# Performance work log

Measured on AMD Instinct MI355X. Metric: run time of the kernel, lower is better.

## Reference

```python
import jax, jax.numpy as jnp
import numpy as np

B, N, C = 4, 8192, 512
H, Dh, G, R = 8, 64, 64, 2  # heads, dim_head, slice_num, mlp_ratio
EPS_LN = 1e-5
EPS_NORM = 1e-5


def _ln(x, g, b):
    m = jnp.mean(x, axis=-1, keepdims=True)
    v = jnp.var(x, axis=-1, keepdims=True)
    return (x - m) * jax.lax.rsqrt(v + EPS_LN) * g + b


def setup_inputs() -> dict:
    key = jax.random.key(0)
    ks = jax.random.split(key, 16)
    r = lambda k, shp: jax.random.normal(k, shp, jnp.float32) * 0.02
    inner = H * Dh
    return {
        "fx": jax.random.normal(ks[0], (B, N, C), jnp.float32),
        "ln1_g": jnp.ones((C,), jnp.float32), "ln1_b": jnp.zeros((C,), jnp.float32),
        "Wx": r(ks[1], (C, inner)), "bx": jnp.zeros((inner,), jnp.float32),
        "Wfx": r(ks[2], (C, inner)), "bfx": jnp.zeros((inner,), jnp.float32),
        "Wslice": r(ks[3], (Dh, G)), "bslice": jnp.zeros((G,), jnp.float32),
        "temperature": jnp.full((1, H, 1, 1), 0.5, jnp.float32),
        "Wq": r(ks[4], (Dh, Dh)), "Wk": r(ks[5], (Dh, Dh)), "Wv": r(ks[6], (Dh, Dh)),
        "Wout": r(ks[7], (inner, C)), "bout": jnp.zeros((C,), jnp.float32),
        "tln_g": jnp.ones((Dh,), jnp.float32), "tln_b": jnp.zeros((Dh,), jnp.float32),
        "Wm1": r(ks[8], (Dh, R * Dh)), "bm1": jnp.zeros((R * Dh,), jnp.float32),
        "Wm2": r(ks[9], (R * Dh, Dh)), "bm2": jnp.zeros((Dh,), jnp.float32),
    }


def reference(fx, ln1_g, ln1_b, Wx, bx, Wfx, bfx, Wslice, bslice, temperature,
              Wq, Wk, Wv, Wout, bout, tln_g, tln_b, Wm1, bm1, Wm2, bm2):
    fx_norm = _ln(fx, ln1_g, ln1_b)                          # [B,N,C]
    # _forward_slice: project to per-head mid features
    x_mid = (fx_norm @ Wx + bx).reshape(B, N, H, Dh).transpose(0, 2, 1, 3)   # [B,H,N,Dh]
    fx_mid = (fx_norm @ Wfx + bfx).reshape(B, N, H, Dh).transpose(0, 2, 1, 3)
    # _project_token: soft slice assignment + weighted pooling into G tokens
    logits = jnp.einsum('bhnd,dg->bhng', x_mid, Wslice) + bslice
    slice_w = jax.nn.softmax(logits / temperature, axis=-1)  # [B,H,N,G]
    slice_norm = jnp.sum(slice_w, axis=2)                    # [B,H,G]
    slice_tok = jnp.einsum('bhnd,bhng->bhgd', fx_mid, slice_w) / (slice_norm[..., None] + EPS_NORM)
    # attention over the small token set (G tokens)
    q = slice_tok @ Wq
    k = slice_tok @ Wk
    v = slice_tok @ Wv
    scale = Dh ** -0.5
    attn = jax.nn.softmax(jnp.einsum('bhgd,bhpd->bhgp', q, k) * scale, axis=-1)
    out_tok = jnp.einsum('bhgp,bhpd->bhgd', attn, v) + slice_tok
    # token MLP with residual
    h = _ln(out_tok, tln_g, tln_b)
    h = jax.nn.gelu(h @ Wm1 + bm1, approximate=False) @ Wm2 + bm2
    tokens = h + out_tok                                     # [B,H,G,Dh]
    # _deslice: weighted scatter back to N points, merge heads, out projection
    out_x = jnp.einsum('bhgd,bhng->bhnd', tokens, slice_w)
    out_x = out_x.transpose(0, 2, 1, 3).reshape(B, N, H * Dh)
    out = out_x @ Wout + bout
    return out + fx_norm
```

## Files before the change

kernel.cpp:

```cpp
#include <hip/hip_runtime.h>
#include <math.h>

#define B_ 4
#define N_ 8192
#define C_ 512
#define H_ 8
#define M_ (B_ * N_)

typedef __attribute__((ext_vector_type(8))) short bf16x8;
typedef __attribute__((ext_vector_type(4))) float f32x4;
typedef __attribute__((ext_vector_type(8))) unsigned short u16x8;
typedef __attribute__((ext_vector_type(4))) unsigned short u16x4;

__device__ __forceinline__ float b2f(unsigned short u) {
  union { unsigned int i; float f; } v;
  v.i = ((unsigned int)u) << 16;
  return v.f;
}
__device__ __forceinline__ unsigned short f2b(float f) {
  union { float f; unsigned int i; } v;
  v.f = f;
  unsigned int r = v.i + 0x7fff + ((v.i >> 16) & 1);
  return (unsigned short)(r >> 16);
}
__device__ __forceinline__ void gl_lds16(const void* g, void* l) {
  __builtin_amdgcn_global_load_lds(
      (const __attribute__((address_space(1))) unsigned int*)g,
      (__attribute__((address_space(3))) unsigned int*)l, 16, 0, 0);
}

__global__ __launch_bounds__(256) void ln_bf16(
    const float* __restrict__ x, const float* __restrict__ gam,
    const float* __restrict__ bet, unsigned short* __restrict__ y) {
  int wave = threadIdx.x >> 6, lane = threadIdx.x & 63;
  int row = (blockIdx.x << 2) + wave;
  const float4* xr = (const float4*)(x + (size_t)row * C_);
  float4 v0 = xr[lane], v1 = xr[lane + 64];
  float s = v0.x + v0.y + v0.z + v0.w + v1.x + v1.y + v1.z + v1.w;
  float q = v0.x * v0.x + v0.y * v0.y + v0.z * v0.z + v0.w * v0.w +
            v1.x * v1.x + v1.y * v1.y + v1.z * v1.z + v1.w * v1.w;
#pragma unroll
  for (int off = 32; off; off >>= 1) {
    s += __shfl_xor(s, off);
    q += __shfl_xor(q, off);
  }
  float mean = s * (1.0f / C_);
  float var = q * (1.0f / C_) - mean * mean;
  float rstd = rsqrtf(var + 1e-5f);
  const float4* gr = (const float4*)gam;
  const float4* br = (const float4*)bet;
  float4 g0 = gr[lane], g1 = gr[lane + 64];
  float4 b0 = br[lane], b1 = br[lane + 64];
  u16x4 oa, ob;
  oa.x = f2b((v0.x - mean) * rstd * g0.x + b0.x);
  oa.y = f2b((v0.y - mean) * rstd * g0.y + b0.y);
  oa.z = f2b((v0.z - mean) * rstd * g0.z + b0.z);
  oa.w = f2b((v0.w - mean) * rstd * g0.w + b0.w);
  ob.x = f2b((v1.x - mean) * rstd * g1.x + b1.x);
  ob.y = f2b((v1.y - mean) * rstd * g1.y + b1.y);
  ob.z = f2b((v1.z - mean) * rstd * g1.z + b1.z);
  ob.w = f2b((v1.w - mean) * rstd * g1.w + b1.w);
  unsigned short* yr = y + (size_t)row * C_;
  *(u16x4*)(yr + (lane << 2)) = oa;
  *(u16x4*)(yr + 256 + (lane << 2)) = ob;
}

__global__ __launch_bounds__(256) void wconv_t(const float* __restrict__ W,
                                               unsigned short* __restrict__ Wt) {
  __shared__ float tile[64][65];
  int t = threadIdx.x;
  int r0 = (int)blockIdx.y << 6, c0 = (int)blockIdx.x << 6;
  int lr = t >> 4, lc = (t & 15) << 2;
#pragma unroll
  for (int p = 0; p < 4; p++) {
    float4 v = *(const float4*)(W + (size_t)(r0 + lr + p * 16) * 512 + c0 + lc);
    tile[lr + p * 16][lc + 0] = v.x;
    tile[lr + p * 16][lc + 1] = v.y;
    tile[lr + p * 16][lc + 2] = v.z;
    tile[lr + p * 16][lc + 3] = v.w;
  }
  __syncthreads();
  int on = t >> 2, ok = (t & 3) << 4;
  unsigned short tmp[16];
#pragma unroll
  for (int j = 0; j < 16; j++) tmp[j] = f2b(tile[ok + j][on]);
  unsigned short* op = Wt + (size_t)(c0 + on) * 512 + r0 + ok;
#pragma unroll
  for (int j4 = 0; j4 < 4; j4++) *(u16x4*)(op + (j4 << 2)) = *(u16x4*)(tmp + (j4 << 2));
}

__global__ __launch_bounds__(256) void wslice_prep(const float* __restrict__ Ws,
                                                   unsigned short* __restrict__ wf) {
  int t = threadIdx.x;
#pragma unroll
  for (int i = 0; i < 2; i++) {
    int idx = t + i * 256;
    int f = idx >> 6, l = idx & 63;
    int gt = f >> 1, ks = f & 1;
    int g = (gt << 4) + (l & 15);
    int d0 = (ks << 5) + ((l >> 4) << 3);
    unsigned short v[8];
#pragma unroll
    for (int jj = 0; jj < 8; jj++) v[jj] = f2b(Ws[(size_t)(d0 + jj) * 64 + g]);
    *(u16x4*)(wf + idx * 8) = *(u16x4*)v;
    *(u16x4*)(wf + idx * 8 + 4) = *(u16x4*)(v + 4);
  }
}

__global__ __launch_bounds__(256) void wfrag_prep(
    const float* __restrict__ Wq, const float* __restrict__ Wk,
    const float* __restrict__ Wv, const float* __restrict__ Wm1,
    const float* __restrict__ Wm2, unsigned short* __restrict__ wfr) {
  int t = threadIdx.x;
  for (int task = t; task < 56 * 64; task += 256) {
    int fid = task >> 6, l = task & 63;
    const float* W;
    int stride, ct, ks;
    if (fid < 24) {
      W = (fid < 8) ? Wq : (fid < 16) ? Wk : Wv;
      int e = fid & 7;
      ct = e >> 1;
      ks = e & 1;
      stride = 64;
    } else if (fid < 40) {
      W = Wm1;
      int e = fid - 24;
      ct = e >> 1;
      ks = e & 1;
      stride = 128;
    } else {
      W = Wm2;
      int e = fid - 40;
      ct = e >> 2;
      ks = e & 3;
      stride = 64;
    }
    int d0 = (ks << 5) + ((l >> 4) << 3);
    int c = (ct << 4) + (l & 15);
    unsigned short v[8];
#pragma unroll
    for (int j = 0; j < 8; j++) v[j] = f2b(W[(size_t)(d0 + j) * stride + c]);
    *(u16x4*)(wfr + task * 8) = *(u16x4*)v;
    *(u16x4*)(wfr + task * 8 + 4) = *(u16x4*)(v + 4);
  }
}

__global__ __launch_bounds__(256) void tokfrag_prep(
    const float* __restrict__ tokens, unsigned short* __restrict__ wtokf) {
  int bh = blockIdx.x, t = threadIdx.x, w = t >> 6, l = t & 63;
  const float* tp = tokens + ((size_t)bh << 12);
#pragma unroll
  for (int fid = w; fid < 8; fid += 4) {
    int mt = fid >> 1, ks = fid & 1;
    int d = (mt << 4) + (l & 15);
    int g0 = (ks << 5) + ((l >> 4) << 3);
    unsigned short v[8];
#pragma unroll
    for (int j = 0; j < 8; j++) v[j] = f2b(tp[(g0 + j) * 64 + d]);
    unsigned short* op = wtokf + (((size_t)bh << 3) + fid) * 512 + (l << 3);
    *(u16x4*)op = *(u16x4*)v;
    *(u16x4*)(op + 4) = *(u16x4*)(v + 4);
  }
}

template <int DEC, bool BIASROW, bool OUTBF, bool RES>
__global__ __launch_bounds__(256) void gemm_bf16(
    const unsigned short* __restrict__ A, const unsigned short* __restrict__ Bt,
    const float* __restrict__ bias, const unsigned short* __restrict__ resid,
    void* __restrict__ Cout, size_t ldC) {
  __shared__ unsigned short lds[8192];
  const int t = threadIdx.x;
  const int w = t >> 6, l = t & 63;
  int bid = blockIdx.x;
  int xcd = bid & 7, q = bid >> 3;
  int bm, bn;
  if (DEC == 0) {
    bm = ((xcd << 5) + (q >> 2)) << 7;
    bn = (q & 3) << 7;
  } else {
    bn = ((xcd << 5) + (q >> 2)) << 7;
    bm = (q & 3) << 7;
  }
  const int wm = (w >> 1) << 6, wn = (w & 1) << 6;
  f32x4 acc[4][4];
#pragma unroll
  for (int mt = 0; mt < 4; mt++)
#pragma unroll
    for (int nt = 0; nt < 4; nt++) acc[mt][nt] = (f32x4){0.f, 0.f, 0.f, 0.f};

  const int srow = t >> 2;
  const int scol = (t & 3) << 3;
  const unsigned short* gA0 = A + (size_t)(bm + srow) * 512 + scol;
  const unsigned short* gA1 = A + (size_t)(bm + 64 + srow) * 512 + scol;
  const unsigned short* gB0 = Bt + (size_t)(bn + srow) * 512 + scol;
  const unsigned short* gB1 = Bt + (size_t)(bn + 64 + srow) * 512 + scol;
  const int fr = l & 15, fq = (l >> 4) << 3;

  for (int k0 = 0; k0 < 512; k0 += 32) {
    gl_lds16(gA0 + k0, lds + (w << 9));
    gl_lds16(gA1 + k0, lds + 2048 + (w << 9));
    gl_lds16(gB0 + k0, lds + 4096 + (w << 9));
    gl_lds16(gB1 + k0, lds + 6144 + (w << 9));
    __syncthreads();
    bf16x8 af[4], bfr[4];
#pragma unroll
    for (int mt = 0; mt < 4; mt++)
      af[mt] = *(const bf16x8*)&lds[(wm + mt * 16 + fr) * 32 + fq];
#pragma unroll
    for (int nt = 0; nt < 4; nt++)
      bfr[nt] = *(const bf16x8*)&lds[4096 + (wn + nt * 16 + fr) * 32 + fq];
#pragma unroll
    for (int mt = 0; mt < 4; mt++)
#pragma unroll
      for (int nt = 0; nt < 4; nt++)
        acc[mt][nt] = __builtin_amdgcn_mfma_f32_16x16x32_bf16(
            af[mt], bfr[nt], acc[mt][nt], 0, 0, 0);
    __syncthreads();
  }

  const int col0 = bn + wn + (l & 15);
  const int row0 = bm + wm + ((l >> 4) << 2);
#pragma unroll
  for (int mt = 0; mt < 4; mt++) {
#pragma unroll
    for (int j = 0; j < 4; j++) {
      int row = row0 + mt * 16 + j;
#pragma unroll
      for (int nt = 0; nt < 4; nt++) {
        int col = col0 + nt * 16;
        float v = acc[mt][nt][j] + (BIASROW ? bias[row] : bias[col]);
        if (RES) v += b2f(resid[(size_t)row * ldC + col]);
        if (OUTBF)
          ((unsigned short*)Cout)[(size_t)row * ldC + col] = f2b(v);
        else
          ((float*)Cout)[(size_t)row * ldC + col] = v;
      }
    }
  }
}

__global__ __launch_bounds__(256) void slice_mfma(
    unsigned short* __restrict__ xw, const unsigned short* __restrict__ wf,
    const float* __restrict__ bslice, const float* __restrict__ temp) {
  __shared__ unsigned short xs[4096];
  int t = threadIdx.x, w = t >> 6, l = t & 63;
  int blk = blockIdx.x;
  size_t base = (size_t)blk << 12;
  {
    int srow = t >> 2;
    const unsigned short* gp = xw + base + srow * 64 + ((t & 3) << 4);
    u16x8 a = *(const u16x8*)gp;
    u16x8 b = *(const u16x8*)(gp + 8);
    int sl0 = (t & 3) << 1, swz = srow & 7;
    *(u16x8*)&xs[srow * 64 + ((sl0 ^ swz) << 3)] = a;
    *(u16x8*)&xs[srow * 64 + (((sl0 + 1) ^ swz) << 3)] = b;
  }
  bf16x8 wsf[4][2];
#pragma unroll
  for (int gt = 0; gt < 4; gt++)
#pragma unroll
    for (int ks = 0; ks < 2; ks++)
      wsf[gt][ks] = *(const bf16x8*)(wf + (((gt << 1) + ks) * 64 + l) * 8);
  __syncthreads();

  int xr = (w << 4) + (l & 15);
  f32x4 acc[4];
#pragma unroll
  for (int gt = 0; gt < 4; gt++) acc[gt] = (f32x4){0.f, 0.f, 0.f, 0.f};
#pragma unroll
  for (int ks = 0; ks < 2; ks++) {
    int slot = (ks << 2) + (l >> 4);
    bf16x8 xf = *(const bf16x8*)&xs[xr * 64 + ((slot ^ (xr & 7)) << 3)];
#pragma unroll
    for (int gt = 0; gt < 4; gt++)
      acc[gt] = __builtin_amdgcn_mfma_f32_16x16x32_bf16(wsf[gt][ks], xf,
                                                        acc[gt], 0, 0, 0);
  }

  int gxr = (blk << 6) + xr;
  float invt = 1.0f / temp[gxr & 7];
  int qq = l >> 4;
  float lg[16];
  float mx = -1e30f;
#pragma unroll
  for (int gt = 0; gt < 4; gt++)
#pragma unroll
    for (int r = 0; r < 4; r++) {
      float v = (acc[gt][r] + bslice[(gt << 4) + (qq << 2) + r]) * invt;
      lg[(gt << 2) + r] = v;
      mx = fmaxf(mx, v);
    }
  mx = fmaxf(mx, __shfl_xor(mx, 16));
  mx = fmaxf(mx, __shfl_xor(mx, 32));
  float ssum = 0.f;
#pragma unroll
  for (int i = 0; i < 16; i++) {
    lg[i] = expf(lg[i] - mx);
    ssum += lg[i];
  }
  ssum += __shfl_xor(ssum, 16);
  ssum += __shfl_xor(ssum, 32);
  float inv = 1.0f / ssum;
  __syncthreads();
#pragma unroll
  for (int gt = 0; gt < 4; gt++) {
    int slot = (gt << 1) + (qq >> 1);
    int off = ((slot ^ (xr & 7)) << 3) + ((qq & 1) << 2);
    u16x4 pk;
    pk.x = f2b(lg[(gt << 2) + 0] * inv);
    pk.y = f2b(lg[(gt << 2) + 1] * inv);
    pk.z = f2b(lg[(gt << 2) + 2] * inv);
    pk.w = f2b(lg[(gt << 2) + 3] * inv);
    *(u16x4*)&xs[xr * 64 + off] = pk;
  }
  __syncthreads();
  {
    int rr = (w << 4) + (l >> 2);
    int sl = (l & 3) << 1, swz = rr & 7;
    u16x8 o0 = *(const u16x8*)&xs[rr * 64 + ((sl ^ swz) << 3)];
    u16x8 o1 = *(const u16x8*)&xs[rr * 64 + (((sl + 1) ^ swz) << 3)];
    unsigned short* op = xw + base + rr * 64 + ((l & 3) << 4);
    *(u16x8*)op = o0;
    *(u16x8*)(op + 8) = o1;
  }
}

__global__ __launch_bounds__(256) void pool_mfma(
    const unsigned short* __restrict__ sw, const unsigned short* __restrict__ fxT,
    float* __restrict__ tok_part, float* __restrict__ norm_part) {
  __shared__ unsigned short wT[4096];
  int bid = blockIdx.x;
  int bh = bid >> 4, c = bid & 15;
  int b = bh >> 3, h = bh & 7;
  int t = threadIdx.x, w = t >> 6, l = t & 63;
  int n0 = c << 9;
  const int fr15 = l & 15, fs = l >> 4;
  f32x4 acc[4];
#pragma unroll
  for (int gt = 0; gt < 4; gt++) acc[gt] = (f32x4){0.f, 0.f, 0.f, 0.f};
  float nacc[4] = {0.f, 0.f, 0.f, 0.f};

  const unsigned short* fxrow =
      fxT + (size_t)(h * 64 + w * 16 + fr15) * 32768 + b * N_ + n0 + (fs << 3);

  for (int nn = 0; nn < 512; nn += 64) {
    size_t srow = ((size_t)(b * N_ + n0 + nn + l) * 8 + h) << 6;
    u16x8 a0 = *(const u16x8*)(sw + srow + w * 16);
    u16x8 a1 = *(const u16x8*)(sw + srow + w * 16 + 8);
    __syncthreads();
#pragma unroll
    for (int j = 0; j < 16; j++) {
      int g = (w << 4) + j;
      unsigned short v = (j < 8) ? (unsigned short)a0[j] : (unsigned short)a1[j - 8];
      wT[(g << 6) + (((l >> 3) ^ (g & 7)) << 3) + (l & 7)] = v;
    }
    __syncthreads();
#pragma unroll
    for (int kk = 0; kk < 2; kk++) {
      bf16x8 bfrag = *(const bf16x8*)(fxrow + nn + (kk << 5));
#pragma unroll
      for (int gt = 0; gt < 4; gt++) {
        int g = (gt << 4) + fr15;
        int slot = (kk << 2) + fs;
        bf16x8 af = *(const bf16x8*)&wT[(g << 6) + ((slot ^ (g & 7)) << 3)];
        acc[gt] = __builtin_amdgcn_mfma_f32_16x16x32_bf16(af, bfrag, acc[gt], 0, 0, 0);
        if (w == 0) {
#pragma unroll
          for (int j = 0; j < 8; j++) nacc[gt] += b2f((unsigned short)af[j]);
        }
      }
    }
  }
  float* op = tok_part + ((size_t)bid << 12);
#pragma unroll
  for (int gt = 0; gt < 4; gt++)
#pragma unroll
    for (int rr = 0; rr < 4; rr++)
      op[((gt << 4) + (fs << 2) + rr) * 64 + (w << 4) + fr15] = acc[gt][rr];
  if (w == 0) {
#pragma unroll
    for (int gt = 0; gt < 4; gt++) {
      float s = nacc[gt];
      s += __shfl_xor(s, 16);
      s += __shfl_xor(s, 32);
      if (l < 16) norm_part[(bid << 6) + (gt << 4) + l] = s;
    }
  }
}

__global__ __launch_bounds__(256) void tok_reduce(
    const float* __restrict__ tok_part, const float* __restrict__ norm_part,
    float* __restrict__ stG) {
  int blk = blockIdx.x;
  int bh = blk >> 2, qq = blk & 3;
  int t = threadIdx.x;
  int e = (qq << 10) + (t << 2);
  int g = e >> 6;
  float s = 0.f;
  const float* np = norm_part + ((size_t)bh << 10);
#pragma unroll
  for (int c = 0; c < 16; c++) s += np[(c << 6) + g];
  float4 acc = make_float4(0.f, 0.f, 0.f, 0.f);
  const float* tp = tok_part + ((size_t)bh << 16) + e;
#pragma unroll
  for (int c = 0; c < 16; c++) {
    float4 v = *(const float4*)(tp + (c << 12));
    acc.x += v.x;
    acc.y += v.y;
    acc.z += v.z;
    acc.w += v.w;
  }
  float inv = 1.0f / (s + 1e-5f);
  acc.x *= inv;
  acc.y *= inv;
  acc.z *= inv;
  acc.w *= inv;
  *(float4*)(stG + ((size_t)bh << 12) + e) = acc;
}

__device__ __forceinline__ float gelu_exact(float x) {
  return 0.5f * x * (1.0f + erff(x * 0.70710678118654752f));
}

__global__ __launch_bounds__(256) void token_mfma(
    const float* __restrict__ stG, const unsigned short* __restrict__ wfr,
    const float* __restrict__ tg, const float* __restrict__ tb,
    const float* __restrict__ bm1, const float* __restrict__ bm2,
    float* __restrict__ tokens) {
  __shared__ __align__(16) char smem[54272];
  unsigned short* stb = (unsigned short*)smem;
  float* st32 = (float*)(smem + 9216);
  unsigned short* hmld = (unsigned short*)(smem + 9216);
  unsigned short* qld = (unsigned short*)(smem + 26624);
  unsigned short* kld = (unsigned short*)(smem + 35840);
  unsigned short* vtl = (unsigned short*)(smem + 45056);

  int bh = blockIdx.x, t = threadIdx.x, w = t >> 6, l = t & 63;
  const int fr = l & 15, fq = l >> 4;

  {
    int r = t >> 2, c0 = (t & 3) << 4;
    const float* gp = stG + ((size_t)bh << 12) + r * 64 + c0;
    float4 a = *(const float4*)gp;
    float4 b = *(const float4*)(gp + 4);
    float4 c = *(const float4*)(gp + 8);
    float4 d = *(const float4*)(gp + 12);
    *(float4*)&st32[r * 68 + c0] = a;
    *(float4*)&st32[r * 68 + c0 + 4] = b;
    *(float4*)&st32[r * 68 + c0 + 8] = c;
    *(float4*)&st32[r * 68 + c0 + 12] = d;
    unsigned short tv[16];
    tv[0] = f2b(a.x); tv[1] = f2b(a.y); tv[2] = f2b(a.z); tv[3] = f2b(a.w);
    tv[4] = f2b(b.x); tv[5] = f2b(b.y); tv[6] = f2b(b.z); tv[7] = f2b(b.w);
    tv[8] = f2b(c.x); tv[9] = f2b(c.y); tv[10] = f2b(c.z); tv[11] = f2b(c.w);
    tv[12] = f2b(d.x); tv[13] = f2b(d.y); tv[14] = f2b(d.z); tv[15] = f2b(d.w);
    *(u16x8*)&stb[r * 72 + c0] = *(u16x8*)tv;
    *(u16x8*)&stb[r * 72 + c0 + 8] = *(u16x8*)(tv + 8);
  }
  __syncthreads();

  const int orow = (w << 4) + (fq << 2);

  {
    bf16x8 af[2];
#pragma unroll
    for (int ks = 0; ks < 2; ks++)
      af[ks] = *(const bf16x8*)&stb[((w << 4) + fr) * 72 + (ks << 5) + (fq << 3)];
    f32x4 aq[4], ak[4], av[4];
#pragma unroll
    for (int ct = 0; ct < 4; ct++) {
      aq[ct] = (f32x4){0.f, 0.f, 0.f, 0.f};
      ak[ct] = (f32x4){0.f, 0.f, 0.f, 0.f};
      av[ct] = (f32x4){0.f, 0.f, 0.f, 0.f};
    }
#pragma unroll
    for (int ct = 0; ct < 4; ct++)
#pragma unroll
      for (int ks = 0; ks < 2; ks++) {
        bf16x8 bq = *(const bf16x8*)&wfr[(((ct << 1) + ks) * 64 + l) * 8];
        aq[ct] = __builtin_amdgcn_mfma_f32_16x16x32_bf16(af[ks], bq, aq[ct], 0, 0, 0);
      }
#pragma unroll
    for (int ct = 0; ct < 4; ct++)
#pragma unroll
      for (int ks = 0; ks < 2; ks++) {
        bf16x8 bk = *(const bf16x8*)&wfr[((8 + (ct << 1) + ks) * 64 + l) * 8];
        ak[ct] = __builtin_amdgcn_mfma_f32_16x16x32_bf16(af[ks], bk, ak[ct], 0, 0, 0);
      }
#pragma unroll
    for (int ct = 0; ct < 4; ct++)
#pragma unroll
      for (int ks = 0; ks < 2; ks++) {
        bf16x8 bv = *(const bf16x8*)&wfr[((16 + (ct << 1) + ks) * 64 + l) * 8];
        av[ct] = __builtin_amdgcn_mfma_f32_16x16x32_bf16(af[ks], bv, av[ct], 0, 0, 0);
      }
#pragma unroll
    for (int ct = 0; ct < 4; ct++) {
#pragma unroll
      for (int rr = 0; rr < 4; rr++) {
        qld[(orow + rr) * 72 + (ct << 4) + fr] = f2b(aq[ct][rr]);
        kld[(orow + rr) * 72 + (ct << 4) + fr] = f2b(ak[ct][rr]);
      }
      u16x4 vp;
      vp.x = f2b(av[ct][0]);
      vp.y = f2b(av[ct][1]);
      vp.z = f2b(av[ct][2]);
      vp.w = f2b(av[ct][3]);
      *(u16x4*)&vtl[((ct << 4) + fr) * 72 + orow] = vp;
    }
  }
  __syncthreads();

  {
    bf16x8 aq[2];
#pragma unroll
    for (int ks = 0; ks < 2; ks++)
      aq[ks] = *(const bf16x8*)&qld[((w << 4) + fr) * 72 + (ks << 5) + (fq << 3)];
    f32x4 accs[4];
#pragma unroll
    for (int nt = 0; nt < 4; nt++) accs[nt] = (f32x4){0.f, 0.f, 0.f, 0.f};
#pragma unroll
    for (int nt = 0; nt < 4; nt++)
#pragma unroll
      for (int ks = 0; ks < 2; ks++) {
        bf16x8 bk = *(const bf16x8*)&kld[((nt << 4) + fr) * 72 + (ks << 5) + (fq << 3)];
        accs[nt] = __builtin_amdgcn_mfma_f32_16x16x32_bf16(aq[ks], bk, accs[nt], 0, 0, 0);
      }
#pragma unroll
    for (int rr = 0; rr < 4; rr++) {
      float v0 = accs[0][rr] * 0.125f, v1 = accs[1][rr] * 0.125f;
      float v2 = accs[2][rr] * 0.125f, v3 = accs[3][rr] * 0.125f;
      float mx = fmaxf(fmaxf(v0, v1), fmaxf(v2, v3));
      mx = fmaxf(mx, __shfl_xor(mx, 1));
      mx = fmaxf(mx, __shfl_xor(mx, 2));
      mx = fmaxf(mx, __shfl_xor(mx, 4));
      mx = fmaxf(mx, __shfl_xor(mx, 8));
      float e0 = expf(v0 - mx), e1 = expf(v1 - mx);
      float e2 = expf(v2 - mx), e3 = expf(v3 - mx);
      float ss = e0 + e1 + e2 + e3;
      ss += __shfl_xor(ss, 1);
      ss += __shfl_xor(ss, 2);
      ss += __shfl_xor(ss, 4);
      ss += __shfl_xor(ss, 8);
      float inv = 1.0f / ss;
      stb[(orow + rr) * 72 + 0 * 16 + fr] = f2b(e0 * inv);
      stb[(orow + rr) * 72 + 1 * 16 + fr] = f2b(e1 * inv);
      stb[(orow + rr) * 72 + 2 * 16 + fr] = f2b(e2 * inv);
      stb[(orow + rr) * 72 + 3 * 16 + fr] = f2b(e3 * inv);
    }
  }
  __syncthreads();

  float o16[4][4];
  {
    bf16x8 ap[2];
#pragma unroll
    for (int ks = 0; ks < 2; ks++)
      ap[ks] = *(const bf16x8*)&stb[((w << 4) + fr) * 72 + (ks << 5) + (fq << 3)];
    f32x4 acco[4];
#pragma unroll
    for (int ct = 0; ct < 4; ct++) acco[ct] = (f32x4){0.f, 0.f, 0.f, 0.f};
#pragma unroll
    for (int ct = 0; ct < 4; ct++)
#pragma unroll
      for (int ks = 0; ks < 2; ks++) {
        bf16x8 bv = *(const bf16x8*)&vtl[((ct << 4) + fr) * 72 + (ks << 5) + (fq << 3)];
        acco[ct] = __builtin_amdgcn_mfma_f32_16x16x32_bf16(ap[ks], bv, acco[ct], 0, 0, 0);
      }
    float tgv[4], tbv[4];
#pragma unroll
    for (int ct = 0; ct < 4; ct++) {
      tgv[ct] = tg[(ct << 4) + fr];
      tbv[ct] = tb[(ct << 4) + fr];
    }
#pragma unroll
    for (int ct = 0; ct < 4; ct++)
#pragma unroll
      for (int rr = 0; rr < 4; rr++)
        o16[ct][rr] = acco[ct][rr] + st32[(orow + rr) * 68 + (ct << 4) + fr];
#pragma unroll
    for (int rr = 0; rr < 4; rr++) {
      float sm = o16[0][rr] + o16[1][rr] + o16[2][rr] + o16[3][rr];
      float sq = o16[0][rr] * o16[0][rr] + o16[1][rr] * o16[1][rr] +
                 o16[2][rr] * o16[2][rr] + o16[3][rr] * o16[3][rr];
      sm += __shfl_xor(sm, 1);
      sm += __shfl_xor(sm, 2);
      sm += __shfl_xor(sm, 4);
      sm += __shfl_xor(sm, 8);
      sq += __shfl_xor(sq, 1);
      sq += __shfl_xor(sq, 2);
      sq += __shfl_xor(sq, 4);
      sq += __shfl_xor(sq, 8);
      float mean = sm * (1.0f / 64.0f);
      float var = sq * (1.0f / 64.0f) - mean * mean;
      float rstd = rsqrtf(var + 1e-5f);
#pragma unroll
      for (int ct = 0; ct < 4; ct++) {
        float hv = (o16[ct][rr] - mean) * rstd * tgv[ct] + tbv[ct];
        qld[(orow + rr) * 72 + (ct << 4) + fr] = f2b(hv);
      }
    }
  }
  __syncthreads();

  {
    bf16x8 ah[2];
#pragma unroll
    for (int ks = 0; ks < 2; ks++)
      ah[ks] = *(const bf16x8*)&qld[((w << 4) + fr) * 72 + (ks << 5) + (fq << 3)];
    f32x4 accm[8];
#pragma unroll
    for (int et = 0; et < 8; et++) accm[et] = (f32x4){0.f, 0.f, 0.f, 0.f};
#pragma unroll
    for (int et = 0; et < 8; et++)
#pragma unroll
      for (int ks = 0; ks < 2; ks++) {
        bf16x8 bm = *(const bf16x8*)&wfr[((24 + (et << 1) + ks) * 64 + l) * 8];
        accm[et] = __builtin_amdgcn_mfma_f32_16x16x32_bf16(ah[ks], bm, accm[et], 0, 0, 0);
      }
#pragma unroll
    for (int et = 0; et < 8; et++) {
      float bv = bm1[(et << 4) + fr];
#pragma unroll
      for (int rr = 0; rr < 4; rr++) {
        float x = accm[et][rr] + bv;
        hmld[(orow + rr) * 136 + (et << 4) + fr] = f2b(gelu_exact(x));
      }
    }
  }
  __syncthreads();

  {
    bf16x8 ahm[4];
#pragma unroll
    for (int ks = 0; ks < 4; ks++)
      ahm[ks] = *(const bf16x8*)&hmld[((w << 4) + fr) * 136 + (ks << 5) + (fq << 3)];
    f32x4 acc2[4];
#pragma unroll
    for (int ct = 0; ct < 4; ct++) acc2[ct] = (f32x4){0.f, 0.f, 0.f, 0.f};
#pragma unroll
    for (int ct = 0; ct < 4; ct++)
#pragma unroll
      for (int ks = 0; ks < 4; ks++) {
        bf16x8 bw = *(const bf16x8*)&wfr[((40 + (ct << 2) + ks) * 64 + l) * 8];
        acc2[ct] = __builtin_amdgcn_mfma_f32_16x16x32_bf16(ahm[ks], bw, acc2[ct], 0, 0, 0);
      }
    float* tout = tokens + ((size_t)bh << 12);
#pragma unroll
    for (int ct = 0; ct < 4; ct++) {
      float bv = bm2[(ct << 4) + fr];
#pragma unroll
      for (int rr = 0; rr < 4; rr++)
        tout[(orow + rr) * 64 + (ct << 4) + fr] = acc2[ct][rr] + bv + o16[ct][rr];
    }
  }
}

__global__ __launch_bounds__(256) void deslice_mfma(
    const unsigned short* __restrict__ wtokf, const unsigned short* __restrict__ sw,
    unsigned short* __restrict__ outx) {
  int bid = blockIdx.x;
  int bh = bid >> 4, c = bid & 15;
  int b = bh >> 3, h = bh & 7;
  int t = threadIdx.x, w = t >> 6, l = t & 63;
  const int fr = l & 15, fq = l >> 4;

  bf16x8 ta[4][2];
  const unsigned short* fp = wtokf + ((size_t)bh << 12);
#pragma unroll
  for (int mt = 0; mt < 4; mt++)
#pragma unroll
    for (int ks = 0; ks < 2; ks++)
      ta[mt][ks] = *(const bf16x8*)(fp + (((mt << 1) + ks) << 9) + (l << 3));

  int n0 = (c << 9) + (w << 7);
#pragma unroll 2
  for (int ntile = 0; ntile < 8; ntile++) {
    int nb = n0 + (ntile << 4);
    size_t rowb = ((size_t)(b * N_ + nb + fr) * 8 + h) << 6;
    bf16x8 b0 = *(const bf16x8*)(sw + rowb + (fq << 3));
    bf16x8 b1 = *(const bf16x8*)(sw + rowb + 32 + (fq << 3));
    f32x4 acc[4];
#pragma unroll
    for (int mt = 0; mt < 4; mt++) acc[mt] = (f32x4){0.f, 0.f, 0.f, 0.f};
#pragma unroll
    for (int mt = 0; mt < 4; mt++) {
      acc[mt] = __builtin_amdgcn_mfma_f32_16x16x32_bf16(ta[mt][0], b0, acc[mt], 0, 0, 0);
      acc[mt] = __builtin_amdgcn_mfma_f32_16x16x32_bf16(ta[mt][1], b1, acc[mt], 0, 0, 0);
    }
    unsigned short* op = outx + rowb + (fq << 2);
#pragma unroll
    for (int mt = 0; mt < 4; mt++) {
      u16x4 pk;
      pk.x = f2b(acc[mt][0]);
      pk.y = f2b(acc[mt][1]);
      pk.z = f2b(acc[mt][2]);
      pk.w = f2b(acc[mt][3]);
      *(u16x4*)(op + (mt << 4)) = pk;
    }
  }
}

extern "C" void kernel_launch(void* const* d_in, const int* in_sizes, int n_in,
                              void* d_out, int out_size, void* d_ws,
                              size_t ws_size, hipStream_t stream) {
  const float* fx = (const float*)d_in[0];
  const float* ln1g = (const float*)d_in[1];
  const float* ln1b = (const float*)d_in[2];
  const float* Wx = (const float*)d_in[3];
  const float* bx = (const float*)d_in[4];
  const float* Wfx = (const float*)d_in[5];
  const float* bfx = (const float*)d_in[6];
  const float* Wsl = (const float*)d_in[7];
  const float* bsl = (const float*)d_in[8];
  const float* temp = (const float*)d_in[9];
  const float* Wq = (const float*)d_in[10];
  const float* Wk = (const float*)d_in[11];
  const float* Wv = (const float*)d_in[12];
  const float* Wout = (const float*)d_in[13];
  const float* bout = (const float*)d_in[14];
  const float* tlng = (const float*)d_in[15];
  const float* tlnb = (const float*)d_in[16];
  const float* Wm1 = (const float*)d_in[17];
  const float* bm1 = (const float*)d_in[18];
  const float* Wm2 = (const float*)d_in[19];
  const float* bm2 = (const float*)d_in[20];
  float* out = (float*)d_out;

  char* p = (char*)d_ws;
  const size_t MC2 = (size_t)M_ * 512 * 2;
  unsigned short* fxn = (unsigned short*)p;  p += MC2;
  unsigned short* buf1 = (unsigned short*)p; p += MC2;
  unsigned short* bufT = (unsigned short*)p; p += MC2;
  unsigned short* WtX = (unsigned short*)p;  p += 512 * 512 * 2;
  unsigned short* WtF = (unsigned short*)p;  p += 512 * 512 * 2;
  unsigned short* WtO = (unsigned short*)p;  p += 512 * 512 * 2;
  unsigned short* wsf = (unsigned short*)p;  p += 8192;
  unsigned short* wfr = (unsigned short*)p;  p += 56 * 512 * 2;
  unsigned short* wtokf = (unsigned short*)p; p += (size_t)32 * 8 * 512 * 2;
  float* tok_part = (float*)p;  p += (size_t)512 * 4096 * 4;
  float* norm_part = (float*)p; p += (size_t)512 * 64 * 4;
  float* tokens = (float*)p;    p += (size_t)32 * 4096 * 4;
  float* stG = (float*)p;       p += (size_t)32 * 4096 * 4;

  ln_bf16<<<M_ / 4, 256, 0, stream>>>(fx, ln1g, ln1b, fxn);
  dim3 wg(8, 8);
  wconv_t<<<wg, 256, 0, stream>>>(Wx, WtX);
  wconv_t<<<wg, 256, 0, stream>>>(Wfx, WtF);
  wconv_t<<<wg, 256, 0, stream>>>(Wout, WtO);
  wslice_prep<<<1, 256, 0, stream>>>(Wsl, wsf);
  wfrag_prep<<<1, 256, 0, stream>>>(Wq, Wk, Wv, Wm1, Wm2, wfr);
  gemm_bf16<0, false, true, false><<<1024, 256, 0, stream>>>(fxn, WtX, bx, nullptr, buf1, 512);
  gemm_bf16<1, true, true, false><<<1024, 256, 0, stream>>>(WtF, fxn, bfx, nullptr, bufT, 32768);
  slice_mfma<<<4096, 256, 0, stream>>>(buf1, wsf, bsl, temp);
  pool_mfma<<<512, 256, 0, stream>>>(buf1, bufT, tok_part, norm_part);
  tok_reduce<<<128, 256, 0, stream>>>(tok_part, norm_part, stG);
  token_mfma<<<32, 256, 0, stream>>>(stG, wfr, tlng, tlnb, bm1, bm2, tokens);
  tokfrag_prep<<<32, 256, 0, stream>>>(tokens, wtokf);
  deslice_mfma<<<512, 256, 0, stream>>>(wtokf, buf1, bufT);
  gemm_bf16<0, false, false, true><<<1024, 256, 0, stream>>>(bufT, WtO, bout, fxn, out, 512);
}
```

Before: 192.9 us.

## Fuse slice softmax into x-projection GEMM, double-buffer GEMM LDS, merge prep kernels

Merges the five weight-preparation launches into a single prep_all kernel. Adds double-buffered LDS staging to the bf16 GEMM so the next K tile is loaded while MFMAs run on the current one. Fuses the slice-logit MFMA and softmax into the epilogue of the x-projection GEMM, so x_mid is never written to and re-read from global memory. In exchange, LDS use per block doubles, which may lower occupancy, and the fused epilogue adds register pressure.

```diff
diff --git a/kernel.cpp b/kernel.cpp
--- a/kernel.cpp
+++ b/kernel.cpp
@@ -65,83 +65,84 @@
   *(u16x4*)(yr + 256 + (lane << 2)) = ob;
 }
 
-__global__ __launch_bounds__(256) void wconv_t(const float* __restrict__ W,
-                                               unsigned short* __restrict__ Wt) {
-  __shared__ float tile[64][65];
-  int t = threadIdx.x;
-  int r0 = (int)blockIdx.y << 6, c0 = (int)blockIdx.x << 6;
-  int lr = t >> 4, lc = (t & 15) << 2;
-#pragma unroll
-  for (int p = 0; p < 4; p++) {
-    float4 v = *(const float4*)(W + (size_t)(r0 + lr + p * 16) * 512 + c0 + lc);
-    tile[lr + p * 16][lc + 0] = v.x;
-    tile[lr + p * 16][lc + 1] = v.y;
-    tile[lr + p * 16][lc + 2] = v.z;
-    tile[lr + p * 16][lc + 3] = v.w;
-  }
-  __syncthreads();
-  int on = t >> 2, ok = (t & 3) << 4;
-  unsigned short tmp[16];
-#pragma unroll
-  for (int j = 0; j < 16; j++) tmp[j] = f2b(tile[ok + j][on]);
-  unsigned short* op = Wt + (size_t)(c0 + on) * 512 + r0 + ok;
-#pragma unroll
-  for (int j4 = 0; j4 < 4; j4++) *(u16x4*)(op + (j4 << 2)) = *(u16x4*)(tmp + (j4 << 2));
-}
-
-__global__ __launch_bounds__(256) void wslice_prep(const float* __restrict__ Ws,
-                                                   unsigned short* __restrict__ wf) {
-  int t = threadIdx.x;
-#pragma unroll
-  for (int i = 0; i < 2; i++) {
-    int idx = t + i * 256;
-    int f = idx >> 6, l = idx & 63;
-    int gt = f >> 1, ks = f & 1;
-    int g = (gt << 4) + (l & 15);
-    int d0 = (ks << 5) + ((l >> 4) << 3);
-    unsigned short v[8];
-#pragma unroll
-    for (int jj = 0; jj < 8; jj++) v[jj] = f2b(Ws[(size_t)(d0 + jj) * 64 + g]);
-    *(u16x4*)(wf + idx * 8) = *(u16x4*)v;
-    *(u16x4*)(wf + idx * 8 + 4) = *(u16x4*)(v + 4);
-  }
-}
-
-__global__ __launch_bounds__(256) void wfrag_prep(
+__global__ __launch_bounds__(256) void prep_all(
+    const float* __restrict__ Wx, const float* __restrict__ Wfx,
+    const float* __restrict__ Wout, const float* __restrict__ Wsl,
     const float* __restrict__ Wq, const float* __restrict__ Wk,
     const float* __restrict__ Wv, const float* __restrict__ Wm1,
-    const float* __restrict__ Wm2, unsigned short* __restrict__ wfr) {
-  int t = threadIdx.x;
-  for (int task = t; task < 56 * 64; task += 256) {
-    int fid = task >> 6, l = task & 63;
-    const float* W;
-    int stride, ct, ks;
-    if (fid < 24) {
-      W = (fid < 8) ? Wq : (fid < 16) ? Wk : Wv;
-      int e = fid & 7;
-      ct = e >> 1;
-      ks = e & 1;
-      stride = 64;
-    } else if (fid < 40) {
-      W = Wm1;
-      int e = fid - 24;
-      ct = e >> 1;
-      ks = e & 1;
-      stride = 128;
-    } else {
-      W = Wm2;
-      int e = fid - 40;
-      ct = e >> 2;
-      ks = e & 3;
-      stride = 64;
-    }
-    int d0 = (ks << 5) + ((l >> 4) << 3);
-    int c = (ct << 4) + (l & 15);
-    unsigned short v[8];
-#pragma unroll
-    for (int j = 0; j < 8; j++) v[j] = f2b(W[(size_t)(d0 + j) * stride + c]);
-    *(u16x4*)(wfr + task * 8) = *(u16x4*)v;
-    *(u16x4*)(wfr + task * 8 + 4) = *(u16x4*)(v + 4);
+    const float* __restrict__ Wm2, unsigned short* __restrict__ WtX,
+    unsigned short* __restrict__ WtF, unsigned short* __restrict__ WtO,
+    unsigned short* __restrict__ wsf, unsigned short* __restrict__ wfr) {
+  __shared__ float tile[64][65];
+  int blk = blockIdx.x, t = threadIdx.x;
+  if (blk < 192) {
+    int which = blk >> 6, sub = blk & 63;
+    const float* W = (which == 0) ? Wx : (which == 1) ? Wfx : Wout;
+    unsigned short* Wt = (which == 0) ? WtX : (which == 1) ? WtF : WtO;
+    int r0 = (sub >> 3) << 6, c0 = (sub & 7) << 6;
+    int lr = t >> 4, lc = (t & 15) << 2;
+#pragma unroll
+    for (int p = 0; p < 4; p++) {
+      float4 v = *(const float4*)(W + (size_t)(r0 + lr + p * 16) * 512 + c0 + lc);
+      tile[lr + p * 16][lc + 0] = v.x;
+      tile[lr + p * 16][lc + 1] = v.y;
+      tile[lr + p * 16][lc + 2] = v.z;
+      tile[lr + p * 16][lc + 3] = v.w;
+    }
+    __syncthreads();
+    int on = t >> 2, ok = (t & 3) << 4;
+    unsigned short tmp[16];
+#pragma unroll
+    for (int j = 0; j < 16; j++) tmp[j] = f2b(tile[ok + j][on]);
+    unsigned short* op = Wt + (size_t)(c0 + on) * 512 + r0 + ok;
+#pragma unroll
+    for (int j4 = 0; j4 < 4; j4++)
+      *(u16x4*)(op + (j4 << 2)) = *(u16x4*)(tmp + (j4 << 2));
+  } else {
+#pragma unroll
+    for (int i = 0; i < 2; i++) {
+      int idx = t + i * 256;
+      int f = idx >> 6, l = idx & 63;
+      int gt = f >> 1, ks = f & 1;
+      int g = (gt << 4) + (l & 15);
+      int d0 = (ks << 5) + ((l >> 4) << 3);
+      unsigned short v[8];
+#pragma unroll
+      for (int jj = 0; jj < 8; jj++) v[jj] = f2b(Wsl[(size_t)(d0 + jj) * 64 + g]);
+      *(u16x4*)(wsf + idx * 8) = *(u16x4*)v;
+      *(u16x4*)(wsf + idx * 8 + 4) = *(u16x4*)(v + 4);
+    }
+    for (int task = t; task < 56 * 64; task += 256) {
+      int fid = task >> 6, l = task & 63;
+      const float* W;
+      int stride, ct, ks;
+      if (fid < 24) {
+        W = (fid < 8) ? Wq : (fid < 16) ? Wk : Wv;
+        int e = fid & 7;
+        ct = e >> 1;
+        ks = e & 1;
+        stride = 64;
+      } else if (fid < 40) {
+        W = Wm1;
+        int e = fid - 24;
+        ct = e >> 1;
+        ks = e & 1;
+        stride = 128;
+      } else {
+        W = Wm2;
+        int e = fid - 40;
+        ct = e >> 2;
+        ks = e & 3;
+        stride = 64;
+      }
+      int d0 = (ks << 5) + ((l >> 4) << 3);
+      int c = (ct << 4) + (l & 15);
+      unsigned short v[8];
+#pragma unroll
+      for (int j = 0; j < 8; j++) v[j] = f2b(W[(size_t)(d0 + j) * stride + c]);
+      *(u16x4*)(wfr + task * 8) = *(u16x4*)v;
+      *(u16x4*)(wfr + task * 8 + 4) = *(u16x4*)(v + 4);
+    }
   }
 }
 
@@ -168,7 +169,7 @@
     const unsigned short* __restrict__ A, const unsigned short* __restrict__ Bt,
     const float* __restrict__ bias, const unsigned short* __restrict__ resid,
     void* __restrict__ Cout, size_t ldC) {
-  __shared__ unsigned short lds[8192];
+  __shared__ unsigned short lds[16384];
   const int t = threadIdx.x;
   const int w = t >> 6, l = t & 63;
   int bid = blockIdx.x;
@@ -196,19 +197,29 @@
   const unsigned short* gB1 = Bt + (size_t)(bn + 64 + srow) * 512 + scol;
   const int fr = l & 15, fq = (l >> 4) << 3;
 
-  for (int k0 = 0; k0 < 512; k0 += 32) {
-    gl_lds16(gA0 + k0, lds + (w << 9));
-    gl_lds16(gA1 + k0, lds + 2048 + (w << 9));
-    gl_lds16(gB0 + k0, lds + 4096 + (w << 9));
-    gl_lds16(gB1 + k0, lds + 6144 + (w << 9));
-    __syncthreads();
+  gl_lds16(gA0, lds + (w << 9));
+  gl_lds16(gA1, lds + 2048 + (w << 9));
+  gl_lds16(gB0, lds + 4096 + (w << 9));
+  gl_lds16(gB1, lds + 6144 + (w << 9));
+  __syncthreads();
+  int cur = 0;
+  for (int ks = 0; ks < 16; ks++) {
+    if (ks < 15) {
+      int k0 = (ks + 1) << 5;
+      unsigned short* st = lds + ((cur ^ 1) << 13);
+      gl_lds16(gA0 + k0, st + (w << 9));
+      gl_lds16(gA1 + k0, st + 2048 + (w << 9));
+      gl_lds16(gB0 + k0, st + 4096 + (w << 9));
+      gl_lds16(gB1 + k0, st + 6144 + (w << 9));
+    }
+    const unsigned short* lb = lds + (cur << 13);
     bf16x8 af[4], bfr[4];
 #pragma unroll
     for (int mt = 0; mt < 4; mt++)
-      af[mt] = *(const bf16x8*)&lds[(wm + mt * 16 + fr) * 32 + fq];
+      af[mt] = *(const bf16x8*)&lb[(wm + mt * 16 + fr) * 32 + fq];
 #pragma unroll
     for (int nt = 0; nt < 4; nt++)
-      bfr[nt] = *(const bf16x8*)&lds[4096 + (wn + nt * 16 + fr) * 32 + fq];
+      bfr[nt] = *(const bf16x8*)&lb[4096 + (wn + nt * 16 + fr) * 32 + fq];
 #pragma unroll
     for (int mt = 0; mt < 4; mt++)
 #pragma unroll
@@ -216,6 +227,7 @@
         acc[mt][nt] = __builtin_amdgcn_mfma_f32_16x16x32_bf16(
             af[mt], bfr[nt], acc[mt][nt], 0, 0, 0);
     __syncthreads();
+    cur ^= 1;
   }
 
   const int col0 = bn + wn + (l & 15);
@@ -239,87 +251,151 @@
   }
 }
 
-__global__ __launch_bounds__(256) void slice_mfma(
-    unsigned short* __restrict__ xw, const unsigned short* __restrict__ wf,
-    const float* __restrict__ bslice, const float* __restrict__ temp) {
-  __shared__ unsigned short xs[4096];
-  int t = threadIdx.x, w = t >> 6, l = t & 63;
-  int blk = blockIdx.x;
-  size_t base = (size_t)blk << 12;
-  {
-    int srow = t >> 2;
-    const unsigned short* gp = xw + base + srow * 64 + ((t & 3) << 4);
-    u16x8 a = *(const u16x8*)gp;
-    u16x8 b = *(const u16x8*)(gp + 8);
-    int sl0 = (t & 3) << 1, swz = srow & 7;
-    *(u16x8*)&xs[srow * 64 + ((sl0 ^ swz) << 3)] = a;
-    *(u16x8*)&xs[srow * 64 + (((sl0 + 1) ^ swz) << 3)] = b;
-  }
+__global__ __launch_bounds__(256) void gemm_slice(
+    const unsigned short* __restrict__ A, const unsigned short* __restrict__ Bt,
+    const float* __restrict__ bias, const unsigned short* __restrict__ wf,
+    const float* __restrict__ bslice, const float* __restrict__ temp,
+    unsigned short* __restrict__ swout) {
+  __shared__ unsigned short lds[16384];
+  const int t = threadIdx.x;
+  const int w = t >> 6, l = t & 63;
+  int bid = blockIdx.x;
+  int xcd = bid & 7, q = bid >> 3;
+  const int bm = ((xcd << 5) + (q >> 2)) << 7;
+  const int bn = (q & 3) << 7;
+  const int wm = (w >> 1) << 6, wn = (w & 1) << 6;
+  f32x4 acc[4][4];
+#pragma unroll
+  for (int mt = 0; mt < 4; mt++)
+#pragma unroll
+    for (int nt = 0; nt < 4; nt++) acc[mt][nt] = (f32x4){0.f, 0.f, 0.f, 0.f};
+
+  const int srow = t >> 2;
+  const int scol = (t & 3) << 3;
+  const unsigned short* gA0 = A + (size_t)(bm + srow) * 512 + scol;
+  const unsigned short* gA1 = A + (size_t)(bm + 64 + srow) * 512 + scol;
+  const unsigned short* gB0 = Bt + (size_t)(bn + srow) * 512 + scol;
+  const unsigned short* gB1 = Bt + (size_t)(bn + 64 + srow) * 512 + scol;
+  const int fr = l & 15, fq = (l >> 4) << 3;
+
+  gl_lds16(gA0, lds + (w << 9));
+  gl_lds16(gA1, lds + 2048 + (w << 9));
+  gl_lds16(gB0, lds + 4096 + (w << 9));
+  gl_lds16(gB1, lds + 6144 + (w << 9));
+  __syncthreads();
+  int cur = 0;
+  for (int ks = 0; ks < 16; ks++) {
+    if (ks < 15) {
+      int k0 = (ks + 1) << 5;
+      unsigned short* st = lds + ((cur ^ 1) << 13);
+      gl_lds16(gA0 + k0, st + (w << 9));
+      gl_lds16(gA1 + k0, st + 2048 + (w << 9));
+      gl_lds16(gB0 + k0, st + 4096 + (w << 9));
+      gl_lds16(gB1 + k0, st + 6144 + (w << 9));
+    }
+    const unsigned short* lb = lds + (cur << 13);
+    bf16x8 af[4], bfr[4];
+#pragma unroll
+    for (int mt = 0; mt < 4; mt++)
+      af[mt] = *(const bf16x8*)&lb[(wm + mt * 16 + fr) * 32 + fq];
+#pragma unroll
+    for (int nt = 0; nt < 4; nt++)
+      bfr[nt] = *(const bf16x8*)&lb[4096 + (wn + nt * 16 + fr) * 32 + fq];
+#pragma unroll
+    for (int mt = 0; mt < 4; mt++)
+#pragma unroll
+      for (int nt = 0; nt < 4; nt++)
+        acc[mt][nt] = __builtin_amdgcn_mfma_f32_16x16x32_bf16(
+            af[mt], bfr[nt], acc[mt][nt], 0, 0, 0);
+    __syncthreads();
+    cur ^= 1;
+  }
+
+  unsigned short* xt = lds + (w << 12);
+  const int h = (bn + wn) >> 6;
+  const int qq = l >> 4;
+#pragma unroll
+  for (int mt = 0; mt < 4; mt++)
+#pragma unroll
+    for (int nt = 0; nt < 4; nt++) {
+      int d = (nt << 4) + fr;
+      float bv = bias[bn + wn + d];
+#pragma unroll
+      for (int j = 0; j < 4; j++) {
+        int r = (mt << 4) + (qq << 2) + j;
+        xt[r * 64 + (((d >> 3) ^ (r & 7)) << 3) + (d & 7)] =
+            f2b(acc[mt][nt][j] + bv);
+      }
+    }
   bf16x8 wsf[4][2];
 #pragma unroll
   for (int gt = 0; gt < 4; gt++)
 #pragma unroll
     for (int ks = 0; ks < 2; ks++)
       wsf[gt][ks] = *(const bf16x8*)(wf + (((gt << 1) + ks) * 64 + l) * 8);
-  __syncthreads();
-
-  int xr = (w << 4) + (l & 15);
-  f32x4 acc[4];
-#pragma unroll
-  for (int gt = 0; gt < 4; gt++) acc[gt] = (f32x4){0.f, 0.f, 0.f, 0.f};
-#pragma unroll
-  for (int ks = 0; ks < 2; ks++) {
-    int slot = (ks << 2) + (l >> 4);
-    bf16x8 xf = *(const bf16x8*)&xs[xr * 64 + ((slot ^ (xr & 7)) << 3)];
+  asm volatile("s_waitcnt lgkmcnt(0)" ::: "memory");
+  __builtin_amdgcn_sched_barrier(0);
+
+  float invt = 1.0f / temp[h];
+#pragma unroll
+  for (int rt = 0; rt < 4; rt++) {
+    int xr = (rt << 4) + fr;
+    f32x4 a4[4];
+#pragma unroll
+    for (int gt = 0; gt < 4; gt++) a4[gt] = (f32x4){0.f, 0.f, 0.f, 0.f};
+#pragma unroll
+    for (int ks = 0; ks < 2; ks++) {
+      int slot = (ks << 2) + qq;
+      bf16x8 xf = *(const bf16x8*)&xt[xr * 64 + ((slot ^ (xr & 7)) << 3)];
+#pragma unroll
+      for (int gt = 0; gt < 4; gt++)
+        a4[gt] = __builtin_amdgcn_mfma_f32_16x16x32_bf16(wsf[gt][ks], xf,
+                                                         a4[gt], 0, 0, 0);
+    }
+    float lg[16];
+    float mx = -1e30f;
 #pragma unroll
     for (int gt = 0; gt < 4; gt++)
-      acc[gt] = __builtin_amdgcn_mfma_f32_16x16x32_bf16(wsf[gt][ks], xf,
-                                                        acc[gt], 0, 0, 0);
-  }
-
-  int gxr = (blk << 6) + xr;
-  float invt = 1.0f / temp[gxr & 7];
-  int qq = l >> 4;
-  float lg[16];
-  float mx = -1e30f;
-#pragma unroll
-  for (int gt = 0; gt < 4; gt++)
-#pragma unroll
-    for (int r = 0; r < 4; r++) {
-      float v = (acc[gt][r] + bslice[(gt << 4) + (qq << 2) + r]) * invt;
-      lg[(gt << 2) + r] = v;
-      mx = fmaxf(mx, v);
-    }
-  mx = fmaxf(mx, __shfl_xor(mx, 16));
-  mx = fmaxf(mx, __shfl_xor(mx, 32));
-  float ssum = 0.f;
-#pragma unroll
-  for (int i = 0; i < 16; i++) {
-    lg[i] = expf(lg[i] - mx);
-    ssum += lg[i];
-  }
-  ssum += __shfl_xor(ssum, 16);
-  ssum += __shfl_xor(ssum, 32);
-  float inv = 1.0f / ssum;
-  __syncthreads();
-#pragma unroll
-  for (int gt = 0; gt < 4; gt++) {
-    int slot = (gt << 1) + (qq >> 1);
-    int off = ((slot ^ (xr & 7)) << 3) + ((qq & 1) << 2);
-    u16x4 pk;
-    pk.x = f2b(lg[(gt << 2) + 0] * inv);
-    pk.y = f2b(lg[(gt << 2) + 1] * inv);
-    pk.z = f2b(lg[(gt << 2) + 2] * inv);
-    pk.w = f2b(lg[(gt << 2) + 3] * inv);
-    *(u16x4*)&xs[xr * 64 + off] = pk;
-  }
-  __syncthreads();
-  {
-    int rr = (w << 4) + (l >> 2);
+#pragma unroll
+      for (int r = 0; r < 4; r++) {
+        float v = (a4[gt][r] + bslice[(gt << 4) + (qq << 2) + r]) * invt;
+        lg[(gt << 2) + r] = v;
+        mx = fmaxf(mx, v);
+      }
+    mx = fmaxf(mx, __shfl_xor(mx, 16));
+    mx = fmaxf(mx, __shfl_xor(mx, 32));
+    float ssum = 0.f;
+#pragma unroll
+    for (int i = 0; i < 16; i++) {
+      lg[i] = expf(lg[i] - mx);
+      ssum += lg[i];
+    }
+    ssum += __shfl_xor(ssum, 16);
+    ssum += __shfl_xor(ssum, 32);
+    float inv = 1.0f / ssum;
+    asm volatile("s_waitcnt lgkmcnt(0)" ::: "memory");
+#pragma unroll
+    for (int gt = 0; gt < 4; gt++) {
+      int slot = (gt << 1) + (qq >> 1);
+      int off = ((slot ^ (xr & 7)) << 3) + ((qq & 1) << 2);
+      u16x4 pk;
+      pk.x = f2b(lg[(gt << 2) + 0] * inv);
+      pk.y = f2b(lg[(gt << 2) + 1] * inv);
+      pk.z = f2b(lg[(gt << 2) + 2] * inv);
+      pk.w = f2b(lg[(gt << 2) + 3] * inv);
+      *(u16x4*)&xt[xr * 64 + off] = pk;
+    }
+  }
+  asm volatile("s_waitcnt lgkmcnt(0)" ::: "memory");
+  __builtin_amdgcn_sched_barrier(0);
+#pragma unroll
+  for (int rt = 0; rt < 4; rt++) {
+    int rr = (rt << 4) + (l >> 2);
     int sl = (l & 3) << 1, swz = rr & 7;
-    u16x8 o0 = *(const u16x8*)&xs[rr * 64 + ((sl ^ swz) << 3)];
-    u16x8 o1 = *(const u16x8*)&xs[rr * 64 + (((sl + 1) ^ swz) << 3)];
-    unsigned short* op = xw + base + rr * 64 + ((l & 3) << 4);
+    u16x8 o0 = *(const u16x8*)&xt[rr * 64 + ((sl ^ swz) << 3)];
+    u16x8 o1 = *(const u16x8*)&xt[rr * 64 + (((sl + 1) ^ swz) << 3)];
+    unsigned short* op =
+        swout + (size_t)(bm + wm + rr) * 512 + (h << 6) + ((l & 3) << 4);
     *(u16x8*)op = o0;
     *(u16x8*)(op + 8) = o1;
   }
@@ -744,15 +820,10 @@
   float* stG = (float*)p;       p += (size_t)32 * 4096 * 4;
 
   ln_bf16<<<M_ / 4, 256, 0, stream>>>(fx, ln1g, ln1b, fxn);
-  dim3 wg(8, 8);
-  wconv_t<<<wg, 256, 0, stream>>>(Wx, WtX);
-  wconv_t<<<wg, 256, 0, stream>>>(Wfx, WtF);
-  wconv_t<<<wg, 256, 0, stream>>>(Wout, WtO);
-  wslice_prep<<<1, 256, 0, stream>>>(Wsl, wsf);
-  wfrag_prep<<<1, 256, 0, stream>>>(Wq, Wk, Wv, Wm1, Wm2, wfr);
-  gemm_bf16<0, false, true, false><<<1024, 256, 0, stream>>>(fxn, WtX, bx, nullptr, buf1, 512);
+  prep_all<<<193, 256, 0, stream>>>(Wx, Wfx, Wout, Wsl, Wq, Wk, Wv, Wm1, Wm2,
+                                    WtX, WtF, WtO, wsf, wfr);
+  gemm_slice<<<1024, 256, 0, stream>>>(fxn, WtX, bx, wsf, bsl, temp, buf1);
   gemm_bf16<1, true, true, false><<<1024, 256, 0, stream>>>(WtF, fxn, bfx, nullptr, bufT, 32768);
-  slice_mfma<<<4096, 256, 0, stream>>>(buf1, wsf, bsl, temp);
   pool_mfma<<<512, 256, 0, stream>>>(buf1, bufT, tok_part, norm_part);
   tok_reduce<<<128, 256, 0, stream>>>(tok_part, norm_part, stG);
   token_mfma<<<32, 256, 0, stream>>>(stG, wfr, tlng, tlnb, bm1, bm2, tokens);
```

New measurement: 194.7 us. About the same (+0.9%).
